# Performance work log

Hardware: AMD Instinct MI355X
Metric: run time of the kernel (lower is better)

The kernel has to match this reference:

```python
import jax, jax.numpy as jnp
import numpy as np

DIM = 1024
HEADS = 16
DIM_HEAD = 64
INNER = HEADS * DIM_HEAD  # 1024
FEAT = 1024  # cfg.different_learnable_tokens=False -> feature_dim = dim
EPS = 1e-5
SCALE = 1.0 / np.sqrt(DIM_HEAD)


def setup_inputs() -> dict:
    key = jax.random.key(0)
    ks = jax.random.split(key, 10)
    b, n = 2, 2048
    x = jax.random.normal(ks[0], (b, n, DIM), jnp.float32)
    y = jax.random.normal(ks[1], (b, n, FEAT), jnp.float32)
    # learned parameters
    ln_g = jnp.ones((DIM,), jnp.float32)
    ln_b = jnp.zeros((DIM,), jnp.float32)
    w_qkv = jax.random.normal(ks[2], (DIM, 3 * INNER), jnp.float32) * (DIM ** -0.5)
    w_av = jax.random.normal(ks[3], (FEAT, INNER), jnp.float32) * (FEAT ** -0.5)
    w_out = jax.random.normal(ks[4], (INNER, DIM), jnp.float32) * (INNER ** -0.5)
    b_out = jnp.zeros((DIM,), jnp.float32)
    w_yout = jax.random.normal(ks[5], (INNER, FEAT), jnp.float32) * (INNER ** -0.5)
    b_yout = jnp.zeros((FEAT,), jnp.float32)
    return {"x": x, "y": y, "ln_g": ln_g, "ln_b": ln_b, "w_qkv": w_qkv,
            "w_av": w_av, "w_out": w_out, "b_out": b_out,
            "w_yout": w_yout, "b_yout": b_yout}


def _split_heads(t):  # [b,n,(h d)] -> [b,h,n,d]
    b, n, _ = t.shape
    return t.reshape(b, n, HEADS, DIM_HEAD).transpose(0, 2, 1, 3)


def _merge_heads(t):  # [b,h,n,d] -> [b,n,(h d)]
    b, h, n, d = t.shape
    return t.transpose(0, 2, 1, 3).reshape(b, n, h * d)


def reference(x, y, ln_g, ln_b, w_qkv, w_av, w_out, b_out, w_yout, b_yout):
    # LayerNorm
    mu = jnp.mean(x, axis=-1, keepdims=True)
    var = jnp.mean(jnp.square(x - mu), axis=-1, keepdims=True)
    xn = (x - mu) * jax.lax.rsqrt(var + EPS) * ln_g + ln_b

    qkv = xn @ w_qkv  # [b,n,3*inner]
    q, k, v = jnp.split(qkv, 3, axis=-1)
    av = y @ w_av  # [b,n,inner]
    q, k, v, av = map(_split_heads, (q, k, v, av))  # [b,h,n,d]

    # shared QK softmax, applied to both V and another_v
    scores = jnp.einsum('bhnd,bhmd->bhnm', q, k) * SCALE
    attn = jax.nn.softmax(scores, axis=-1)
    x_ctx = jnp.einsum('bhnm,bhmd->bhnd', attn, v)
    y_ctx = jnp.einsum('bhnm,bhmd->bhnd', attn, av)

    x_out = _merge_heads(x_ctx) @ w_out + b_out
    y_out = _merge_heads(y_ctx) @ w_yout + b_yout
    return (x_out, y_out)
```

## Files before the change

### kernel.cpp

```cpp
#include <hip/hip_runtime.h>

typedef _Float16 half8 __attribute__((ext_vector_type(8)));
typedef _Float16 half4v __attribute__((ext_vector_type(4)));
typedef float f32x4 __attribute__((ext_vector_type(4)));
typedef unsigned int u32;

#define SEQ 2048
#define NTOK 4096
#define DM 1024
#define QKS 2048
#define LN_EPS 1e-5f
#define LOG2E_SCALE 0.18033688f

typedef const __attribute__((address_space(1))) u32* gas_ptr;
typedef __attribute__((address_space(3))) u32* las_ptr;
__device__ __forceinline__ void gld_lds16(const void* g, void* l) {
  __builtin_amdgcn_global_load_lds((gas_ptr)g, (las_ptr)l, 16, 0, 0);
}

#define BARRIER() do { __builtin_amdgcn_s_barrier(); __builtin_amdgcn_sched_barrier(0); } while (0)
#define VMW(N) do { asm volatile("s_waitcnt vmcnt(" #N ")" ::: "memory"); __builtin_amdgcn_sched_barrier(0); } while (0)
#define LGW() do { asm volatile("s_waitcnt lgkmcnt(0)" ::: "memory"); __builtin_amdgcn_sched_barrier(0); } while (0)

__global__ __launch_bounds__(256) void prep_kernel(
    const float* __restrict__ x, const float* __restrict__ g, const float* __restrict__ bta,
    const float* __restrict__ y,
    const float* __restrict__ w_qkv, const float* __restrict__ w_av,
    const float* __restrict__ w_out, const float* __restrict__ w_yout,
    _Float16* __restrict__ xn, _Float16* __restrict__ yh,
    _Float16* __restrict__ wqkvT, _Float16* __restrict__ wavT,
    _Float16* __restrict__ woutT, _Float16* __restrict__ wyoutT) {
  __shared__ float smem[64 * 65];
  const int bid = blockIdx.x;
  const int t = threadIdx.x;
  if (bid < 4096) {
    const int row = bid;
    const float4 v = ((const float4*)(x + (size_t)row * DM))[t];
    float s = v.x + v.y + v.z + v.w;
#pragma unroll
    for (int m = 1; m < 64; m <<= 1) s += __shfl_xor(s, m, 64);
    float* red = smem;
    const int wid = t >> 6, lane = t & 63;
    if (lane == 0) red[wid] = s;
    __syncthreads();
    const float mu = (red[0] + red[1] + red[2] + red[3]) * (1.0f / DM);
    const float dx = v.x - mu, dy = v.y - mu, dz = v.z - mu, dw = v.w - mu;
    float ss = dx * dx + dy * dy + dz * dz + dw * dw;
#pragma unroll
    for (int m = 1; m < 64; m <<= 1) ss += __shfl_xor(ss, m, 64);
    __syncthreads();
    if (lane == 0) red[wid] = ss;
    __syncthreads();
    const float var = (red[0] + red[1] + red[2] + red[3]) * (1.0f / DM);
    const float rstd = rsqrtf(var + LN_EPS);
    const float4 gg = ((const float4*)g)[t];
    const float4 bb = ((const float4*)bta)[t];
    half4v o;
    o[0] = (_Float16)(dx * rstd * gg.x + bb.x);
    o[1] = (_Float16)(dy * rstd * gg.y + bb.y);
    o[2] = (_Float16)(dz * rstd * gg.z + bb.z);
    o[3] = (_Float16)(dw * rstd * gg.w + bb.w);
    *(half4v*)(xn + (size_t)row * DM + t * 4) = o;
  } else if (bid < 8192) {
    const int row = bid - 4096;
    const float4 v = ((const float4*)(y + (size_t)row * DM))[t];
    half4v o;
    o[0] = (_Float16)v.x; o[1] = (_Float16)v.y;
    o[2] = (_Float16)v.z; o[3] = (_Float16)v.w;
    *(half4v*)(yh + (size_t)row * DM + t * 4) = o;
  } else {
    const int id2 = bid - 8192;
    const float* W; _Float16* WT; int Nc, bx, by;
    if (id2 < 768) { W = w_qkv; WT = wqkvT; Nc = 3072; bx = id2 % 48; by = id2 / 48; }
    else {
      const int id3 = id2 - 768, sel = id3 >> 8;
      Nc = 1024; bx = id3 & 15; by = (id3 >> 4) & 15;
      if (sel == 0) { W = w_av; WT = wavT; }
      else if (sel == 1) { W = w_out; WT = woutT; }
      else { W = w_yout; WT = wyoutT; }
    }
    float (*tile)[65] = (float(*)[65])smem;
    const int n0 = bx * 64, k0 = by * 64;
    const int c = t & 63;
#pragma unroll
    for (int i = 0; i < 16; i++) {
      const int r = (t >> 6) * 16 + i;
      tile[r][c] = W[(size_t)(k0 + r) * Nc + n0 + c];
    }
    __syncthreads();
#pragma unroll
    for (int i = 0; i < 16; i++) {
      const int n = (t >> 6) * 16 + i;
      WT[(size_t)(n0 + n) * 1024 + k0 + c] = (_Float16)tile[c][n];
    }
  }
}

__global__ __launch_bounds__(512, 2) void gemm8p_kernel(
    const _Float16* __restrict__ xn, const _Float16* __restrict__ wqkvT,
    const _Float16* __restrict__ yh, const _Float16* __restrict__ wavT,
    _Float16* __restrict__ qkvm, _Float16* __restrict__ vtb,
    _Float16* __restrict__ avtb) {
  __shared__ _Float16 Ab[2][8192];
  __shared__ _Float16 Bb[2][8192];
  const int swz = ((blockIdx.x & 7) << 5) + (blockIdx.x >> 3);
  const _Float16 *A, *B;
  int m0, n0, isav;
  if (swz < 192) { A = xn; B = wqkvT; m0 = (swz / 12) * 256; n0 = (swz % 12) * 256; isav = 0; }
  else { const int u = swz - 192; A = yh; B = wavT; m0 = (u >> 2) * 256; n0 = (u & 3) * 256; isav = 1; }
  const int t = threadIdx.x;
  const int wid = t >> 6, lane = t & 63, lo = lane & 15, hi = lane >> 4;
  const int wm = wid >> 2, wn = wid & 3;
  const int srow = t >> 2;
  const int sx = ((t & 3) ^ (srow & 3)) << 3;
  const _Float16* gA = A + (size_t)(m0 + srow) * 1024 + sx;
  const _Float16* gB = B + (size_t)(n0 + srow) * 1024 + sx;
  const int rdz = (hi ^ (lo & 3)) << 3;
  const int arow = (wm * 128 + lo) * 32 + rdz;
  const int brow = (wn * 64 + lo) * 32 + rdz;

  f32x4 acc[8][4];
#pragma unroll
  for (int i = 0; i < 8; i++)
#pragma unroll
    for (int j = 0; j < 4; j++) {
      acc[i][j][0] = 0.f; acc[i][j][1] = 0.f; acc[i][j][2] = 0.f; acc[i][j][3] = 0.f;
    }
  half8 af[4], bf[4];

#define STG_A(BUF, HH, KT) gld_lds16(gA + (HH) * 131072 + (KT) * 32, &Ab[BUF][(HH) * 4096 + t * 8])
#define STG_B(BUF, HH, KT) gld_lds16(gB + (HH) * 131072 + (KT) * 32, &Bb[BUF][(HH) * 4096 + t * 8])
#define RDA(BUF, FB)                                                     \
  _Pragma("unroll") for (int f2 = 0; f2 < 4; f2++)                       \
      af[f2] = *(const half8*)&Ab[BUF][arow + ((FB) + f2) * 512]
#define RDB(BUF, G0)                                                     \
  _Pragma("unroll") for (int g2 = 0; g2 < 2; g2++)                       \
      bf[(G0) + g2] = *(const half8*)&Bb[BUF][brow + ((G0) + g2) * 512]
#define MMA(FB, G0)                                                      \
  do {                                                                   \
    __builtin_amdgcn_s_setprio(1);                                       \
    _Pragma("unroll") for (int f2 = 0; f2 < 4; f2++)                     \
        _Pragma("unroll") for (int g2 = 0; g2 < 2; g2++)                 \
            acc[(FB) + f2][(G0) + g2] = __builtin_amdgcn_mfma_f32_16x16x32_f16( \
                af[f2], bf[(G0) + g2], acc[(FB) + f2][(G0) + g2], 0, 0, 0); \
    __builtin_amdgcn_s_setprio(0);                                       \
  } while (0)

  STG_A(0, 0, 0); STG_A(0, 1, 0); STG_B(0, 0, 0); STG_B(0, 1, 0);
  STG_A(1, 0, 1);

  for (int it = 0; it < 16; it++) {
    const int T1 = 2 * it + 1;
    const int N0 = (2 * it + 2) & 31, N1 = (2 * it + 3) & 31;
    VMW(1); BARRIER();
    RDA(0, 0); RDB(0, 0);
    STG_A(1, 1, T1);
    LGW(); MMA(0, 0);
    BARRIER(); RDB(0, 2); STG_B(1, 0, T1); LGW(); MMA(0, 2);
    BARRIER(); RDA(0, 4); STG_B(1, 1, T1); LGW(); MMA(4, 2);
    BARRIER(); STG_A(0, 0, N0); MMA(4, 0);
    VMW(1); BARRIER();
    RDA(1, 0); RDB(1, 0);
    STG_A(0, 1, N0);
    LGW(); MMA(0, 0);
    BARRIER(); RDB(1, 2); STG_B(0, 0, N0); LGW(); MMA(0, 2);
    BARRIER(); RDA(1, 4); STG_B(0, 1, N0); LGW(); MMA(4, 2);
    BARRIER(); STG_A(1, 0, N1); MMA(4, 0);
  }
#undef STG_A
#undef STG_B
#undef RDA
#undef RDB
#undef MMA

#pragma unroll
  for (int f = 0; f < 8; f++)
#pragma unroll
    for (int g = 0; g < 4; g++)
#pragma unroll
      for (int r = 0; r < 4; r++) {
        const int row = m0 + wm * 128 + f * 16 + 4 * hi + r;
        const int col = n0 + wn * 64 + g * 16 + lo;
        const _Float16 v = (_Float16)acc[f][g][r];
        if (!isav && col < 2048) {
          qkvm[(size_t)row * QKS + col] = v;
        } else {
          const int coff = isav ? col : col - 2048;
          _Float16* Ct = isav ? avtb : vtb;
          Ct[(((size_t)((row >> 11) << 4) + (coff >> 6)) * 64 + (coff & 63)) * SEQ +
             (row & (SEQ - 1))] = v;
        }
      }
}

__global__ __launch_bounds__(512, 2) void gemmout8p_kernel(
    const _Float16* __restrict__ xc, const _Float16* __restrict__ woutT,
    float* __restrict__ o0, const float* __restrict__ b0,
    const _Float16* __restrict__ yc, const _Float16* __restrict__ wyoutT,
    float* __restrict__ o1, const float* __restrict__ b1) {
  __shared__ _Float16 Ab[2][8192];
  __shared__ _Float16 Bb[2][8192];
  const int swz = ((blockIdx.x & 7) << 4) + (blockIdx.x >> 3);
  const _Float16 *A, *B;
  float* F; const float* bias;
  int u;
  if (swz < 64) { A = xc; B = woutT; F = o0; bias = b0; u = swz; }
  else { A = yc; B = wyoutT; F = o1; bias = b1; u = swz - 64; }
  const int m0 = (u >> 2) * 256, n0 = (u & 3) * 256;
  const int t = threadIdx.x;
  const int wid = t >> 6, lane = t & 63, lo = lane & 15, hi = lane >> 4;
  const int wm = wid >> 2, wn = wid & 3;
  const int srow = t >> 2;
  const int sx = ((t & 3) ^ (srow & 3)) << 3;
  const _Float16* gA = A + (size_t)(m0 + srow) * 1024 + sx;
  const _Float16* gB = B + (size_t)(n0 + srow) * 1024 + sx;
  const int rdz = (hi ^ (lo & 3)) << 3;
  const int arow = (wm * 128 + lo) * 32 + rdz;
  const int brow = (wn * 64 + lo) * 32 + rdz;

  f32x4 acc[8][4];
#pragma unroll
  for (int i = 0; i < 8; i++)
#pragma unroll
    for (int j = 0; j < 4; j++) {
      acc[i][j][0] = 0.f; acc[i][j][1] = 0.f; acc[i][j][2] = 0.f; acc[i][j][3] = 0.f;
    }
  half8 af[4], bf[4];

#define STG_A(BUF, HH, KT) gld_lds16(gA + (HH) * 131072 + (KT) * 32, &Ab[BUF][(HH) * 4096 + t * 8])
#define STG_B(BUF, HH, KT) gld_lds16(gB + (HH) * 131072 + (KT) * 32, &Bb[BUF][(HH) * 4096 + t * 8])
#define RDA(BUF, FB)                                                     \
  _Pragma("unroll") for (int f2 = 0; f2 < 4; f2++)                       \
      af[f2] = *(const half8*)&Ab[BUF][arow + ((FB) + f2) * 512]
#define RDB(BUF, G0)                                                     \
  _Pragma("unroll") for (int g2 = 0; g2 < 2; g2++)                       \
      bf[(G0) + g2] = *(const half8*)&Bb[BUF][brow + ((G0) + g2) * 512]
#define MMA(FB, G0)                                                      \
  do {                                                                   \
    __builtin_amdgcn_s_setprio(1);                                       \
    _Pragma("unroll") for (int f2 = 0; f2 < 4; f2++)                     \
        _Pragma("unroll") for (int g2 = 0; g2 < 2; g2++)                 \
            acc[(FB) + f2][(G0) + g2] = __builtin_amdgcn_mfma_f32_16x16x32_f16( \
                af[f2], bf[(G0) + g2], acc[(FB) + f2][(G0) + g2], 0, 0, 0); \
    __builtin_amdgcn_s_setprio(0);                                       \
  } while (0)

  STG_A(0, 0, 0); STG_A(0, 1, 0); STG_B(0, 0, 0); STG_B(0, 1, 0);
  STG_A(1, 0, 1);

  for (int it = 0; it < 16; it++) {
    const int T1 = 2 * it + 1;
    const int N0 = (2 * it + 2) & 31, N1 = (2 * it + 3) & 31;
    VMW(1); BARRIER();
    RDA(0, 0); RDB(0, 0);
    STG_A(1, 1, T1);
    LGW(); MMA(0, 0);
    BARRIER(); RDB(0, 2); STG_B(1, 0, T1); LGW(); MMA(0, 2);
    BARRIER(); RDA(0, 4); STG_B(1, 1, T1); LGW(); MMA(4, 2);
    BARRIER(); STG_A(0, 0, N0); MMA(4, 0);
    VMW(1); BARRIER();
    RDA(1, 0); RDB(1, 0);
    STG_A(0, 1, N0);
    LGW(); MMA(0, 0);
    BARRIER(); RDB(1, 2); STG_B(0, 0, N0); LGW(); MMA(0, 2);
    BARRIER(); RDA(1, 4); STG_B(0, 1, N0); LGW(); MMA(4, 2);
    BARRIER(); STG_A(1, 0, N1); MMA(4, 0);
  }
#undef STG_A
#undef STG_B
#undef RDA
#undef RDB
#undef MMA

#pragma unroll
  for (int f = 0; f < 8; f++)
#pragma unroll
    for (int g = 0; g < 4; g++)
#pragma unroll
      for (int r = 0; r < 4; r++) {
        const int row = m0 + wm * 128 + f * 16 + 4 * hi + r;
        const int col = n0 + wn * 64 + g * 16 + lo;
        F[(size_t)row * 1024 + col] = acc[f][g][r] + bias[col];
      }
}

__global__ __launch_bounds__(256) void attn_kernel(
    const _Float16* __restrict__ qkvm,
    const _Float16* __restrict__ vt,
    const _Float16* __restrict__ avt,
    _Float16* __restrict__ xctx, _Float16* __restrict__ yctx) {
  __shared__ _Float16 Kl[2][4096];
  __shared__ _Float16 Vl[4096];
  __shared__ _Float16 Al[4096];
  __shared__ _Float16 Pl[4][2048];

  const int t = threadIdx.x;
  const int wid = t >> 6, lane = t & 63, lo = lane & 15, hi = lane >> 4;
  const int l7 = lane & 7;
  const int id = blockIdx.x;
  const int bh = ((id & 7) << 2) + ((id >> 3) >> 4);
  const int qt = (id >> 3) & 15;
  const int b = bh >> 4, h = bh & 15;
  const int q0 = qt * 128 + wid * 32;
  const size_t tokbase = (size_t)b * SEQ;
  const _Float16* vbase = vt + (size_t)bh * 64 * SEQ;
  const _Float16* abase = avt + (size_t)bh * 64 * SEQ;
  _Float16* Pw = Pl[wid];
  const int NT = SEQ / 64;

  half8 qf[2][2];
#pragma unroll
  for (int rg = 0; rg < 2; rg++)
#pragma unroll
    for (int kc = 0; kc < 2; kc++)
      qf[rg][kc] = *(const half8*)(qkvm + (tokbase + q0 + rg * 16 + lo) * QKS +
                                   h * 64 + kc * 32 + hi * 8);

  f32x4 zero;
  zero[0] = 0.f; zero[1] = 0.f; zero[2] = 0.f; zero[3] = 0.f;
  f32x4 accx[2][4], accy[2][4];
  float mC[2], lsum[2];
#pragma unroll
  for (int rg = 0; rg < 2; rg++) {
#pragma unroll
    for (int j = 0; j < 4; j++) { accx[rg][j] = zero; accy[rg][j] = zero; }
    mC[rg] = -1.0e30f; lsum[rg] = 0.0f;
  }

  const int skey = t >> 3;
  const int sc7 = t & 7;

#define STAGE_K(kv0, BSEL)                                                        \
  do {                                                                            \
    _Pragma("unroll") for (int j = 0; j < 2; j++) {                               \
      const int key = skey + j * 32;                                              \
      const int cs = ((sc7 ^ (key & 7)) << 3);                                    \
      gld_lds16(qkvm + (tokbase + (kv0) + key) * QKS + DM + h * 64 + cs,          \
                &Kl[BSEL][j * 2048 + wid * 512]);                                 \
    }                                                                             \
  } while (0)

  half8 vreg[2], areg[2];
#define LOAD_VA(kv0)                                                              \
  do {                                                                            \
    _Pragma("unroll") for (int j = 0; j < 2; j++) {                               \
      const int drow = skey + j * 32;                                             \
      const int cs = ((sc7 ^ (drow & 7)) << 3);                                   \
      vreg[j] = *(const half8*)(vbase + (size_t)drow * SEQ + (kv0) + cs);         \
      areg[j] = *(const half8*)(abase + (size_t)drow * SEQ + (kv0) + cs);         \
    }                                                                             \
  } while (0)

#define WRITE_VA()                                                                \
  do {                                                                            \
    _Pragma("unroll") for (int j = 0; j < 2; j++) {                               \
      *(half8*)(Vl + j * 2048 + t * 8) = vreg[j];                                 \
      *(half8*)(Al + j * 2048 + t * 8) = areg[j];                                 \
    }                                                                             \
  } while (0)

  STAGE_K(0, 0);
#pragma unroll
  for (int j = 0; j < 2; j++) {
    const int drow = skey + j * 32;
    const int cs = ((sc7 ^ (drow & 7)) << 3);
    gld_lds16(vbase + (size_t)drow * SEQ + cs, &Vl[j * 2048 + wid * 512]);
    gld_lds16(abase + (size_t)drow * SEQ + cs, &Al[j * 2048 + wid * 512]);
  }
  LOAD_VA(64);

  for (int tt = 0; tt < NT; tt++) {
    if (tt + 1 < NT) { VMW(4); } else { VMW(0); }
    BARRIER();
    if (tt + 1 < NT) STAGE_K((tt + 1) * 64, (tt & 1) ^ 1);
    const _Float16* Kb = Kl[tt & 1];

    f32x4 s[2][4];
#pragma unroll
    for (int kg = 0; kg < 4; kg++) {
      const int kr = (kg * 16 + lo) * 64;
      const half8 ak0 = *(const half8*)(Kb + kr + ((hi ^ l7) << 3));
      const half8 ak1 = *(const half8*)(Kb + kr + (((4 | hi) ^ l7) << 3));
#pragma unroll
      for (int rg = 0; rg < 2; rg++) {
        f32x4 z = __builtin_amdgcn_mfma_f32_16x16x32_f16(ak0, qf[rg][0], zero, 0, 0, 0);
        s[rg][kg] = __builtin_amdgcn_mfma_f32_16x16x32_f16(ak1, qf[rg][1], z, 0, 0, 0);
      }
    }

    float tmC[2];
#pragma unroll
    for (int rg = 0; rg < 2; rg++) {
      float tm = -3.0e38f;
#pragma unroll
      for (int kg = 0; kg < 4; kg++)
#pragma unroll
        for (int r = 0; r < 4; r++) tm = fmaxf(tm, s[rg][kg][r]);
      tm = fmaxf(tm, __shfl_xor(tm, 16, 64));
      tm = fmaxf(tm, __shfl_xor(tm, 32, 64));
      tmC[rg] = tm * LOG2E_SCALE;
    }

    const bool grow = (tmC[0] > mC[0] + 8.0f) | (tmC[1] > mC[1] + 8.0f);
    if (__any(grow)) {
      float fcs[2];
#pragma unroll
      for (int rg = 0; rg < 2; rg++) {
        const float mn = fmaxf(mC[rg], tmC[rg]);
        fcs[rg] = exp2f(mC[rg] - mn);
        mC[rg] = mn;
        lsum[rg] *= fcs[rg];
      }
#pragma unroll
      for (int rg = 0; rg < 2; rg++)
#pragma unroll
        for (int r = 0; r < 4; r++) {
          const float fcb = __shfl(fcs[rg], 4 * hi + r, 64);
#pragma unroll
          for (int ng = 0; ng < 4; ng++) {
            accx[rg][ng][r] *= fcb;
            accy[rg][ng][r] *= fcb;
          }
        }
    }

#pragma unroll
    for (int rg = 0; rg < 2; rg++) {
      float rs = 0.0f;
#pragma unroll
      for (int kg = 0; kg < 4; kg++) {
        half4v pk;
#pragma unroll
        for (int r = 0; r < 4; r++) {
          const float p = exp2f(fmaf(s[rg][kg][r], LOG2E_SCALE, -mC[rg]));
          rs += p;
          pk[r] = (_Float16)p;
        }
        *(half4v*)(Pw + (rg * 16 + lo) * 64 +
                   (((kg * 2 + (hi >> 1)) ^ l7) << 3) + ((hi & 1) << 2)) = pk;
      }
      rs += __shfl_xor(rs, 16, 64);
      rs += __shfl_xor(rs, 32, 64);
      lsum[rg] += rs;
    }

#pragma unroll
    for (int kk = 0; kk < 2; kk++) {
      half8 pa[2];
#pragma unroll
      for (int rg = 0; rg < 2; rg++)
        pa[rg] = *(const half8*)(Pw + (rg * 16 + lo) * 64 + (((kk * 4 + hi) ^ l7) << 3));
#pragma unroll
      for (int ng = 0; ng < 4; ng++) {
        const int vr = (ng * 16 + lo) * 64 + (((kk * 4 + hi) ^ l7) << 3);
        const half8 bv = *(const half8*)(Vl + vr);
        const half8 ba = *(const half8*)(Al + vr);
#pragma unroll
        for (int rg = 0; rg < 2; rg++) {
          accx[rg][ng] = __builtin_amdgcn_mfma_f32_16x16x32_f16(pa[rg], bv, accx[rg][ng], 0, 0, 0);
          accy[rg][ng] = __builtin_amdgcn_mfma_f32_16x16x32_f16(pa[rg], ba, accy[rg][ng], 0, 0, 0);
        }
      }
    }

    if (tt + 1 < NT) {
      VMW(2);
      BARRIER();
      WRITE_VA();
      LGW();
      if (tt + 2 < NT) LOAD_VA((tt + 2) * 64);
    }
  }
#undef STAGE_K
#undef LOAD_VA
#undef WRITE_VA

#pragma unroll
  for (int rg = 0; rg < 2; rg++) {
    const float inv = 1.0f / lsum[rg];
#pragma unroll
    for (int r = 0; r < 4; r++) {
      const float invb = __shfl(inv, 4 * hi + r, 64);
      const size_t tok = tokbase + q0 + rg * 16 + 4 * hi + r;
#pragma unroll
      for (int ng = 0; ng < 4; ng++) {
        const int col = h * 64 + ng * 16 + lo;
        xctx[tok * DM + col] = (_Float16)(accx[rg][ng][r] * invb);
        yctx[tok * DM + col] = (_Float16)(accy[rg][ng][r] * invb);
      }
    }
  }
}

extern "C" void kernel_launch(void* const* d_in, const int* in_sizes, int n_in,
                              void* d_out, int out_size, void* d_ws, size_t ws_size,
                              hipStream_t stream) {
  const float* x      = (const float*)d_in[0];
  const float* y      = (const float*)d_in[1];
  const float* ln_g   = (const float*)d_in[2];
  const float* ln_b   = (const float*)d_in[3];
  const float* w_qkv  = (const float*)d_in[4];
  const float* w_av   = (const float*)d_in[5];
  const float* w_out  = (const float*)d_in[6];
  const float* b_out  = (const float*)d_in[7];
  const float* w_yout = (const float*)d_in[8];
  const float* b_yout = (const float*)d_in[9];
  float* out = (float*)d_out;

  _Float16* ws     = (_Float16*)d_ws;
  _Float16* xn     = ws;
  _Float16* yh     = xn + 4194304;
  _Float16* wqkvT  = yh + 4194304;
  _Float16* wavT   = wqkvT + 3145728;
  _Float16* woutT  = wavT + 1048576;
  _Float16* wyoutT = woutT + 1048576;
  _Float16* qkvm   = wyoutT + 1048576;
  _Float16* vtb    = qkvm + 8388608;
  _Float16* avtb   = vtb + 4194304;
  _Float16* xc     = avtb + 4194304;
  _Float16* yc     = xc + 4194304;

  prep_kernel<<<9728, 256, 0, stream>>>(x, ln_g, ln_b, y, w_qkv, w_av, w_out, w_yout,
                                        xn, yh, wqkvT, wavT, woutT, wyoutT);

  gemm8p_kernel<<<256, 512, 0, stream>>>(xn, wqkvT, yh, wavT, qkvm, vtb, avtb);

  attn_kernel<<<512, 256, 0, stream>>>(qkvm, vtb, avtb, xc, yc);

  gemmout8p_kernel<<<128, 512, 0, stream>>>(
      xc, woutT, out, b_out,
      yc, wyoutT, out + 4194304, b_yout);
}
```

Baseline: 242.1 us.

## Shrink attention tiles to 16 queries per wave and 32-key double-buffered stages

```diff
diff --git a/kernel.cpp b/kernel.cpp
--- a/kernel.cpp
+++ b/kernel.cpp
@@ -284,210 +284,148 @@
       }
 }
 
-__global__ __launch_bounds__(256) void attn_kernel(
+__global__ __launch_bounds__(256, 4) void attn_kernel(
     const _Float16* __restrict__ qkvm,
     const _Float16* __restrict__ vt,
     const _Float16* __restrict__ avt,
     _Float16* __restrict__ xctx, _Float16* __restrict__ yctx) {
-  __shared__ _Float16 Kl[2][4096];
-  __shared__ _Float16 Vl[4096];
-  __shared__ _Float16 Al[4096];
-  __shared__ _Float16 Pl[4][2048];
+  __shared__ _Float16 Kl[2][2048];
+  __shared__ _Float16 Vl[2][2048];
+  __shared__ _Float16 Al[2][2048];
+  __shared__ _Float16 Pl[4][512];
 
   const int t = threadIdx.x;
   const int wid = t >> 6, lane = t & 63, lo = lane & 15, hi = lane >> 4;
-  const int l7 = lane & 7;
   const int id = blockIdx.x;
-  const int bh = ((id & 7) << 2) + ((id >> 3) >> 4);
-  const int qt = (id >> 3) & 15;
+  const int bh = ((id & 7) << 2) + ((id >> 3) >> 5);
+  const int qt = (id >> 3) & 31;
   const int b = bh >> 4, h = bh & 15;
-  const int q0 = qt * 128 + wid * 32;
+  const int q0 = qt * 64 + wid * 16;
   const size_t tokbase = (size_t)b * SEQ;
   const _Float16* vbase = vt + (size_t)bh * 64 * SEQ;
   const _Float16* abase = avt + (size_t)bh * 64 * SEQ;
   _Float16* Pw = Pl[wid];
-  const int NT = SEQ / 64;
-
-  half8 qf[2][2];
-#pragma unroll
-  for (int rg = 0; rg < 2; rg++)
-#pragma unroll
-    for (int kc = 0; kc < 2; kc++)
-      qf[rg][kc] = *(const half8*)(qkvm + (tokbase + q0 + rg * 16 + lo) * QKS +
-                                   h * 64 + kc * 32 + hi * 8);
+  const int NT = SEQ / 32;
+  const int swzP = (lo & 3) ^ ((lo >> 2) & 3);
+
+  half8 qf[2];
+#pragma unroll
+  for (int kc = 0; kc < 2; kc++)
+    qf[kc] = *(const half8*)(qkvm + (tokbase + q0 + lo) * QKS +
+                             h * 64 + kc * 32 + hi * 8);
 
   f32x4 zero;
   zero[0] = 0.f; zero[1] = 0.f; zero[2] = 0.f; zero[3] = 0.f;
-  f32x4 accx[2][4], accy[2][4];
-  float mC[2], lsum[2];
-#pragma unroll
-  for (int rg = 0; rg < 2; rg++) {
-#pragma unroll
-    for (int j = 0; j < 4; j++) { accx[rg][j] = zero; accy[rg][j] = zero; }
-    mC[rg] = -1.0e30f; lsum[rg] = 0.0f;
-  }
-
-  const int skey = t >> 3;
-  const int sc7 = t & 7;
-
-#define STAGE_K(kv0, BSEL)                                                        \
+  f32x4 accx[4], accy[4];
+  float mC = -1.0e30f, lsum = 0.0f;
+#pragma unroll
+  for (int j = 0; j < 4; j++) { accx[j] = zero; accy[j] = zero; }
+
+  const int kkey = t >> 3, kc7 = t & 7;
+  const int vrow = t >> 2, vc3 = t & 3;
+  const int kcs = ((kc7 ^ (kkey & 7)) << 3);
+  const int vcs = ((vc3 ^ ((vrow & 3) ^ ((vrow >> 2) & 3))) << 3);
+
+#define STAGE(kv0, BSEL)                                                          \
   do {                                                                            \
-    _Pragma("unroll") for (int j = 0; j < 2; j++) {                               \
-      const int key = skey + j * 32;                                              \
-      const int cs = ((sc7 ^ (key & 7)) << 3);                                    \
-      gld_lds16(qkvm + (tokbase + (kv0) + key) * QKS + DM + h * 64 + cs,          \
-                &Kl[BSEL][j * 2048 + wid * 512]);                                 \
-    }                                                                             \
+    gld_lds16(qkvm + (tokbase + (kv0) + kkey) * QKS + DM + h * 64 + kcs,          \
+              &Kl[BSEL][(t >> 6) * 512 + (t & 63) * 8]);                          \
+    gld_lds16(vbase + (size_t)vrow * SEQ + (kv0) + vcs,                           \
+              &Vl[BSEL][(t >> 6) * 512 + (t & 63) * 8]);                          \
+    gld_lds16(abase + (size_t)vrow * SEQ + (kv0) + vcs,                           \
+              &Al[BSEL][(t >> 6) * 512 + (t & 63) * 8]);                          \
   } while (0)
 
-  half8 vreg[2], areg[2];
-#define LOAD_VA(kv0)                                                              \
-  do {                                                                            \
-    _Pragma("unroll") for (int j = 0; j < 2; j++) {                               \
-      const int drow = skey + j * 32;                                             \
-      const int cs = ((sc7 ^ (drow & 7)) << 3);                                   \
-      vreg[j] = *(const half8*)(vbase + (size_t)drow * SEQ + (kv0) + cs);         \
-      areg[j] = *(const half8*)(abase + (size_t)drow * SEQ + (kv0) + cs);         \
-    }                                                                             \
-  } while (0)
-
-#define WRITE_VA()                                                                \
-  do {                                                                            \
-    _Pragma("unroll") for (int j = 0; j < 2; j++) {                               \
-      *(half8*)(Vl + j * 2048 + t * 8) = vreg[j];                                 \
-      *(half8*)(Al + j * 2048 + t * 8) = areg[j];                                 \
-    }                                                                             \
-  } while (0)
-
-  STAGE_K(0, 0);
-#pragma unroll
-  for (int j = 0; j < 2; j++) {
-    const int drow = skey + j * 32;
-    const int cs = ((sc7 ^ (drow & 7)) << 3);
-    gld_lds16(vbase + (size_t)drow * SEQ + cs, &Vl[j * 2048 + wid * 512]);
-    gld_lds16(abase + (size_t)drow * SEQ + cs, &Al[j * 2048 + wid * 512]);
-  }
-  LOAD_VA(64);
-
+  STAGE(0, 0);
+  int bsel = 0;
   for (int tt = 0; tt < NT; tt++) {
-    if (tt + 1 < NT) { VMW(4); } else { VMW(0); }
-    BARRIER();
-    if (tt + 1 < NT) STAGE_K((tt + 1) * 64, (tt & 1) ^ 1);
-    const _Float16* Kb = Kl[tt & 1];
-
-    f32x4 s[2][4];
-#pragma unroll
-    for (int kg = 0; kg < 4; kg++) {
-      const int kr = (kg * 16 + lo) * 64;
-      const half8 ak0 = *(const half8*)(Kb + kr + ((hi ^ l7) << 3));
-      const half8 ak1 = *(const half8*)(Kb + kr + (((4 | hi) ^ l7) << 3));
-#pragma unroll
-      for (int rg = 0; rg < 2; rg++) {
-        f32x4 z = __builtin_amdgcn_mfma_f32_16x16x32_f16(ak0, qf[rg][0], zero, 0, 0, 0);
-        s[rg][kg] = __builtin_amdgcn_mfma_f32_16x16x32_f16(ak1, qf[rg][1], z, 0, 0, 0);
+    __syncthreads();
+    if (tt + 1 < NT) STAGE((tt + 1) * 32, bsel ^ 1);
+    const _Float16* Kb = Kl[bsel];
+    const _Float16* Vb = Vl[bsel];
+    const _Float16* Ab = Al[bsel];
+
+    f32x4 s[2];
+#pragma unroll
+    for (int kg = 0; kg < 2; kg++) {
+      const int krow = kg * 16 + lo;
+      const int kr = krow * 64;
+      const half8 ak0 = *(const half8*)(Kb + kr + ((hi ^ (krow & 7)) << 3));
+      const half8 ak1 = *(const half8*)(Kb + kr + (((4 | hi) ^ (krow & 7)) << 3));
+      f32x4 z = __builtin_amdgcn_mfma_f32_16x16x32_f16(ak0, qf[0], zero, 0, 0, 0);
+      s[kg] = __builtin_amdgcn_mfma_f32_16x16x32_f16(ak1, qf[1], z, 0, 0, 0);
+    }
+
+    float tm = -3.0e38f;
+#pragma unroll
+    for (int kg = 0; kg < 2; kg++)
+#pragma unroll
+      for (int r = 0; r < 4; r++) tm = fmaxf(tm, s[kg][r]);
+    tm = fmaxf(tm, __shfl_xor(tm, 16, 64));
+    tm = fmaxf(tm, __shfl_xor(tm, 32, 64));
+    const float tmC = tm * LOG2E_SCALE;
+
+    if (__any(tmC > mC + 8.0f)) {
+      const float mn = fmaxf(mC, tmC);
+      const float fcs = exp2f(mC - mn);
+      mC = mn;
+      lsum *= fcs;
+#pragma unroll
+      for (int r = 0; r < 4; r++) {
+        const float fcb = __shfl(fcs, 4 * hi + r, 64);
+#pragma unroll
+        for (int ng = 0; ng < 4; ng++) {
+          accx[ng][r] *= fcb;
+          accy[ng][r] *= fcb;
+        }
       }
     }
 
-    float tmC[2];
-#pragma unroll
-    for (int rg = 0; rg < 2; rg++) {
-      float tm = -3.0e38f;
-#pragma unroll
-      for (int kg = 0; kg < 4; kg++)
-#pragma unroll
-        for (int r = 0; r < 4; r++) tm = fmaxf(tm, s[rg][kg][r]);
-      tm = fmaxf(tm, __shfl_xor(tm, 16, 64));
-      tm = fmaxf(tm, __shfl_xor(tm, 32, 64));
-      tmC[rg] = tm * LOG2E_SCALE;
-    }
-
-    const bool grow = (tmC[0] > mC[0] + 8.0f) | (tmC[1] > mC[1] + 8.0f);
-    if (__any(grow)) {
-      float fcs[2];
-#pragma unroll
-      for (int rg = 0; rg < 2; rg++) {
-        const float mn = fmaxf(mC[rg], tmC[rg]);
-        fcs[rg] = exp2f(mC[rg] - mn);
-        mC[rg] = mn;
-        lsum[rg] *= fcs[rg];
-      }
-#pragma unroll
-      for (int rg = 0; rg < 2; rg++)
+    {
+      float rs = 0.0f;
+#pragma unroll
+      for (int kg = 0; kg < 2; kg++) {
+        half4v pk;
 #pragma unroll
         for (int r = 0; r < 4; r++) {
-          const float fcb = __shfl(fcs[rg], 4 * hi + r, 64);
-#pragma unroll
-          for (int ng = 0; ng < 4; ng++) {
-            accx[rg][ng][r] *= fcb;
-            accy[rg][ng][r] *= fcb;
-          }
-        }
-    }
-
-#pragma unroll
-    for (int rg = 0; rg < 2; rg++) {
-      float rs = 0.0f;
-#pragma unroll
-      for (int kg = 0; kg < 4; kg++) {
-        half4v pk;
-#pragma unroll
-        for (int r = 0; r < 4; r++) {
-          const float p = exp2f(fmaf(s[rg][kg][r], LOG2E_SCALE, -mC[rg]));
+          const float p = exp2f(fmaf(s[kg][r], LOG2E_SCALE, -mC));
           rs += p;
           pk[r] = (_Float16)p;
         }
-        *(half4v*)(Pw + (rg * 16 + lo) * 64 +
-                   (((kg * 2 + (hi >> 1)) ^ l7) << 3) + ((hi & 1) << 2)) = pk;
+        *(half4v*)(Pw + lo * 32 +
+                   (((kg * 2 + (hi >> 1)) ^ swzP) << 3) + ((hi & 1) << 2)) = pk;
       }
       rs += __shfl_xor(rs, 16, 64);
       rs += __shfl_xor(rs, 32, 64);
-      lsum[rg] += rs;
-    }
-
-#pragma unroll
-    for (int kk = 0; kk < 2; kk++) {
-      half8 pa[2];
-#pragma unroll
-      for (int rg = 0; rg < 2; rg++)
-        pa[rg] = *(const half8*)(Pw + (rg * 16 + lo) * 64 + (((kk * 4 + hi) ^ l7) << 3));
+      lsum += rs;
+    }
+
+    {
+      const half8 pa = *(const half8*)(Pw + lo * 32 + ((hi ^ swzP) << 3));
 #pragma unroll
       for (int ng = 0; ng < 4; ng++) {
-        const int vr = (ng * 16 + lo) * 64 + (((kk * 4 + hi) ^ l7) << 3);
-        const half8 bv = *(const half8*)(Vl + vr);
-        const half8 ba = *(const half8*)(Al + vr);
-#pragma unroll
-        for (int rg = 0; rg < 2; rg++) {
-          accx[rg][ng] = __builtin_amdgcn_mfma_f32_16x16x32_f16(pa[rg], bv, accx[rg][ng], 0, 0, 0);
-          accy[rg][ng] = __builtin_amdgcn_mfma_f32_16x16x32_f16(pa[rg], ba, accy[rg][ng], 0, 0, 0);
-        }
+        const int vrow2 = ng * 16 + lo;
+        const int vr = vrow2 * 32 + ((hi ^ ((vrow2 & 3) ^ ((vrow2 >> 2) & 3))) << 3);
+        const half8 bv = *(const half8*)(Vb + vr);
+        const half8 ba = *(const half8*)(Ab + vr);
+        accx[ng] = __builtin_amdgcn_mfma_f32_16x16x32_f16(pa, bv, accx[ng], 0, 0, 0);
+        accy[ng] = __builtin_amdgcn_mfma_f32_16x16x32_f16(pa, ba, accy[ng], 0, 0, 0);
       }
     }
-
-    if (tt + 1 < NT) {
-      VMW(2);
-      BARRIER();
-      WRITE_VA();
-      LGW();
-      if (tt + 2 < NT) LOAD_VA((tt + 2) * 64);
-    }
+    bsel ^= 1;
   }
-#undef STAGE_K
-#undef LOAD_VA
-#undef WRITE_VA
-
-#pragma unroll
-  for (int rg = 0; rg < 2; rg++) {
-    const float inv = 1.0f / lsum[rg];
-#pragma unroll
-    for (int r = 0; r < 4; r++) {
-      const float invb = __shfl(inv, 4 * hi + r, 64);
-      const size_t tok = tokbase + q0 + rg * 16 + 4 * hi + r;
-#pragma unroll
-      for (int ng = 0; ng < 4; ng++) {
-        const int col = h * 64 + ng * 16 + lo;
-        xctx[tok * DM + col] = (_Float16)(accx[rg][ng][r] * invb);
-        yctx[tok * DM + col] = (_Float16)(accy[rg][ng][r] * invb);
-      }
+#undef STAGE
+
+  const float inv = 1.0f / lsum;
+#pragma unroll
+  for (int r = 0; r < 4; r++) {
+    const float invb = __shfl(inv, 4 * hi + r, 64);
+    const size_t tok = tokbase + q0 + 4 * hi + r;
+#pragma unroll
+    for (int ng = 0; ng < 4; ng++) {
+      const int col = h * 64 + ng * 16 + lo;
+      xctx[tok * DM + col] = (_Float16)(accx[ng][r] * invb);
+      yctx[tok * DM + col] = (_Float16)(accy[ng][r] * invb);
     }
   }
 }
@@ -525,7 +463,7 @@
 
   gemm8p_kernel<<<256, 512, 0, stream>>>(xn, wqkvT, yh, wavT, qkvm, vtb, avtb);
 
-  attn_kernel<<<512, 256, 0, stream>>>(qkvm, vtb, avtb, xc, yc);
+  attn_kernel<<<1024, 256, 0, stream>>>(qkvm, vtb, avtb, xc, yc);
 
   gemmout8p_kernel<<<128, 512, 0, stream>>>(
       xc, woutT, out, b_out,
```

Measured after the change: 210.7 us. -13.0%, faster.
